# Performance work log

Measured on AMD Instinct MI355X. Metric: run time of the kernel, lower is better.

## Reference

```python
import jax, jax.numpy as jnp
import numpy as np


def setup_inputs() -> dict:
    key = jax.random.key(0)
    k1, k2 = jax.random.split(key)
    TOKENS, IN_F, OUT_F = 8192, 4096, 4096
    x = jax.random.normal(k1, (TOKENS, IN_F), dtype=jnp.float32)
    # kaiming_uniform_(a=sqrt(5)) then *2.0 -> roughly uniform in [-2/sqrt(in), 2/sqrt(in)]
    bound = 2.0 / np.sqrt(IN_F)
    weight = jax.random.uniform(k2, (OUT_F, IN_F), dtype=jnp.float32,
                                minval=-bound, maxval=bound)
    alpha = jnp.asarray(0.1, dtype=jnp.float32)
    bias = jnp.zeros((OUT_F,), dtype=jnp.float32)
    return {"x": x, "weight": weight, "alpha": alpha, "bias": bias, "bitwidth": 2}


def _quantize(W, alpha_eff, bitwidth):
    # alpha_eff > 0 scalar; W: [out, in]
    Wa = W / alpha_eff
    Wc = jnp.clip(Wa, -1.0, 1.0)
    if bitwidth == 1:
        Q = jnp.sign(Wc)
        Q = jnp.where(Q == 0, 1.0, Q)  # sign(0) -> +1
    elif bitwidth == 2:
        Q = jnp.where(jnp.abs(Wc) < 0.5, 0.0, jnp.sign(Wc))
    else:
        raise ValueError("bitwidth must be 1 or 2 here")
    return alpha_eff * Q


def reference(x, weight, alpha, bias, bitwidth):
    if bitwidth == 32:
        W_used = weight
    else:
        alpha_eff = jnp.abs(alpha) + 1e-8
        W_used = _quantize(weight, alpha_eff, bitwidth)
    # F.linear: x @ W^T + b
    return jnp.dot(x, W_used.T) + bias
```

## Files before the change

kernel.cpp:

```cpp
#include <hip/hip_runtime.h>


__global__ void qlin_row_flags(const float* __restrict__ W,
                               const float* __restrict__ alpha,
                               const int* __restrict__ bitwidth,
                               int* __restrict__ flags,
                               int IN_F) {
    const int row = blockIdx.x;
    const int bw = *bitwidth;
    __shared__ int s_any;
    if (threadIdx.x == 0) s_any = 0;
    __syncthreads();

    if (bw != 2) {
        if (threadIdx.x == 0) flags[row] = 1;
        return;
    }

    const float alpha_eff = fabsf(*alpha) + 1e-8f;
    bool any = false;

    const size_t base = (size_t)row * (size_t)IN_F;
    const int n4 = IN_F >> 2;
    const float4* Wrow4 = (const float4*)(W + base);
    for (int i = threadIdx.x; i < n4; i += blockDim.x) {
        float4 w = Wrow4[i];
        float ax = fabsf(fminf(1.f, fmaxf(-1.f, w.x / alpha_eff)));
        float ay = fabsf(fminf(1.f, fmaxf(-1.f, w.y / alpha_eff)));
        float az = fabsf(fminf(1.f, fmaxf(-1.f, w.z / alpha_eff)));
        float aw = fabsf(fminf(1.f, fmaxf(-1.f, w.w / alpha_eff)));
        any |= (ax >= 0.5f) | (ay >= 0.5f) | (az >= 0.5f) | (aw >= 0.5f);
    }
    for (int i = (n4 << 2) + threadIdx.x; i < IN_F; i += blockDim.x) {
        float a = fabsf(fminf(1.f, fmaxf(-1.f, W[base + i] / alpha_eff)));
        any |= (a >= 0.5f);
    }

    if (any) s_any = 1;
    __syncthreads();
    if (threadIdx.x == 0) flags[row] = s_any;
}

__global__ void qlin_output(const float* __restrict__ x,
                            const float* __restrict__ W,
                            const float* __restrict__ alpha,
                            const float* __restrict__ bias,
                            const int* __restrict__ bitwidth,
                            const int* __restrict__ flags,
                            float* __restrict__ y,
                            int TOKENS, int IN_F, int OUT_F) {
    const int per_tok_blocks = OUT_F >> 10;
    const int t  = blockIdx.x / per_tok_blocks;
    const int j0 = (blockIdx.x % per_tok_blocks) * 1024 + threadIdx.x * 4;
    if (t >= TOKENS || j0 + 3 >= OUT_F) return;

    const int4   f = *(const int4*)(flags + j0);
    const float4 b = *(const float4*)(bias + j0);
    float* yp = y + (size_t)t * (size_t)OUT_F + j0;

    if ((f.x | f.y | f.z | f.w) == 0) {
        *(float4*)yp = b;
        return;
    }

    const int bw = *bitwidth;
    const float alpha_eff = fabsf(*alpha) + 1e-8f;
    float acc[4] = {0.f, 0.f, 0.f, 0.f};
    const float* xr = x + (size_t)t * (size_t)IN_F;
    for (int i = 0; i < IN_F; ++i) {
        const float xv = xr[i];
#pragma unroll
        for (int c = 0; c < 4; ++c) {
            float w = W[(size_t)(j0 + c) * (size_t)IN_F + i];
            float wu;
            if (bw == 32) {
                wu = w;
            } else {
                float wa = fminf(1.f, fmaxf(-1.f, w / alpha_eff));
                float q;
                if (bw == 1) {
                    q = (wa >= 0.f) ? 1.f : -1.f;
                } else {
                    q = (fabsf(wa) < 0.5f) ? 0.f : ((wa > 0.f) ? 1.f : -1.f);
                }
                wu = alpha_eff * q;
            }
            acc[c] = fmaf(xv, wu, acc[c]);
        }
    }
    *(float4*)yp = make_float4(acc[0] + b.x, acc[1] + b.y,
                               acc[2] + b.z, acc[3] + b.w);
}

extern "C" void kernel_launch(void* const* d_in, const int* in_sizes, int n_in,
                              void* d_out, int out_size, void* d_ws, size_t ws_size,
                              hipStream_t stream) {
    const float* x     = (const float*)d_in[0];
    const float* W     = (const float*)d_in[1];
    const float* alpha = (const float*)d_in[2];
    const float* bias  = (const float*)d_in[3];
    const int*   bw    = (const int*)d_in[4];

    const int OUT_F  = in_sizes[3];
    const int IN_F   = in_sizes[1] / OUT_F;
    const int TOKENS = in_sizes[0] / IN_F;

    float* y = (float*)d_out;
    int* flags = (int*)d_ws;

    qlin_row_flags<<<OUT_F, 256, 0, stream>>>(W, alpha, bw, flags, IN_F);

    const int per_tok_blocks = OUT_F >> 10;
    dim3 grid(TOKENS * per_tok_blocks);
    qlin_output<<<grid, 256, 0, stream>>>(x, W, alpha, bias, bw, flags, y,
                                          TOKENS, IN_F, OUT_F);
}
```

Measured before the change: 243.6 us.

## Fuse row-flag scan and output pass into one column-blocked kernel

Merges the per-row zero-check kernel and the output kernel into a single launch. Each 1024-thread block scans 16 weight rows, keeps the flags in shared memory, then loops over all tokens to write either the bias or a dot product for those columns. The flag test now compares |w| against 0.5*alpha instead of dividing each weight, and the global flag workspace goes away. The cost is only 256 blocks with a serial scan-then-write phase, and output stores become 64-byte strided chunks per token row, which may weaken write coalescing.

Result: slower. 269.7 us (+10.7%).

```diff
diff --git a/kernel.cpp b/kernel.cpp
--- a/kernel.cpp
+++ b/kernel.cpp
@@ -1,95 +1,92 @@
 #include <hip/hip_runtime.h>
 
 
-__global__ void qlin_row_flags(const float* __restrict__ W,
-                               const float* __restrict__ alpha,
-                               const int* __restrict__ bitwidth,
-                               int* __restrict__ flags,
-                               int IN_F) {
-    const int row = blockIdx.x;
-    const int bw = *bitwidth;
-    __shared__ int s_any;
-    if (threadIdx.x == 0) s_any = 0;
+#define COLS_PER_BLOCK 16
+
+__global__ __launch_bounds__(1024) void qlin_fused(
+    const float* __restrict__ x,
+    const float* __restrict__ W,
+    const float* __restrict__ alpha,
+    const float* __restrict__ bias,
+    const int* __restrict__ bitwidth,
+    float* __restrict__ y,
+    int TOKENS, int IN_F, int OUT_F)
+{
+    const int j0  = blockIdx.x * COLS_PER_BLOCK;
+    const int tid = threadIdx.x;
+    const int bw  = *bitwidth;
+
+    __shared__ int s_flags[COLS_PER_BLOCK];
+
+    if (bw != 2) {
+        if (tid < COLS_PER_BLOCK) s_flags[tid] = 1;
+    } else {
+        if (tid < COLS_PER_BLOCK) s_flags[tid] = 0;
+        __syncthreads();
+        const float alpha_eff = fabsf(*alpha) + 1e-8f;
+        const float thr = 0.5f * alpha_eff;
+        const int n4 = IN_F >> 2;
+#pragma unroll
+        for (int k = 0; k < COLS_PER_BLOCK; ++k) {
+            const float4* Wrow = (const float4*)(W + (size_t)(j0 + k) * IN_F);
+            bool any = false;
+            for (int i = tid; i < n4; i += 1024) {
+                float4 w = Wrow[i];
+                any |= (fabsf(w.x) >= thr) | (fabsf(w.y) >= thr) |
+                       (fabsf(w.z) >= thr) | (fabsf(w.w) >= thr);
+            }
+            for (int i = (n4 << 2) + tid; i < IN_F; i += 1024)
+                any |= (fabsf(W[(size_t)(j0 + k) * IN_F + i]) >= thr);
+            if (any) s_flags[k] = 1;
+        }
+    }
     __syncthreads();
 
-    if (bw != 2) {
-        if (threadIdx.x == 0) flags[row] = 1;
-        return;
-    }
+    const int cg = tid & 3;
+    const int ts = tid >> 2;
+    const int c0 = cg << 2;
+    const int dense = s_flags[c0] | s_flags[c0 + 1] | s_flags[c0 + 2] | s_flags[c0 + 3];
+    const float4 bv = *(const float4*)(bias + j0 + c0);
 
-    const float alpha_eff = fabsf(*alpha) + 1e-8f;
-    bool any = false;
-
-    const size_t base = (size_t)row * (size_t)IN_F;
-    const int n4 = IN_F >> 2;
-    const float4* Wrow4 = (const float4*)(W + base);
-    for (int i = threadIdx.x; i < n4; i += blockDim.x) {
-        float4 w = Wrow4[i];
-        float ax = fabsf(fminf(1.f, fmaxf(-1.f, w.x / alpha_eff)));
-        float ay = fabsf(fminf(1.f, fmaxf(-1.f, w.y / alpha_eff)));
-        float az = fabsf(fminf(1.f, fmaxf(-1.f, w.z / alpha_eff)));
-        float aw = fabsf(fminf(1.f, fmaxf(-1.f, w.w / alpha_eff)));
-        any |= (ax >= 0.5f) | (ay >= 0.5f) | (az >= 0.5f) | (aw >= 0.5f);
-    }
-    for (int i = (n4 << 2) + threadIdx.x; i < IN_F; i += blockDim.x) {
-        float a = fabsf(fminf(1.f, fmaxf(-1.f, W[base + i] / alpha_eff)));
-        any |= (a >= 0.5f);
-    }
-
-    if (any) s_any = 1;
-    __syncthreads();
-    if (threadIdx.x == 0) flags[row] = s_any;
-}
-
-__global__ void qlin_output(const float* __restrict__ x,
-                            const float* __restrict__ W,
-                            const float* __restrict__ alpha,
-                            const float* __restrict__ bias,
-                            const int* __restrict__ bitwidth,
-                            const int* __restrict__ flags,
-                            float* __restrict__ y,
-                            int TOKENS, int IN_F, int OUT_F) {
-    const int per_tok_blocks = OUT_F >> 10;
-    const int t  = blockIdx.x / per_tok_blocks;
-    const int j0 = (blockIdx.x % per_tok_blocks) * 1024 + threadIdx.x * 4;
-    if (t >= TOKENS || j0 + 3 >= OUT_F) return;
-
-    const int4   f = *(const int4*)(flags + j0);
-    const float4 b = *(const float4*)(bias + j0);
-    float* yp = y + (size_t)t * (size_t)OUT_F + j0;
-
-    if ((f.x | f.y | f.z | f.w) == 0) {
-        *(float4*)yp = b;
-        return;
-    }
-
-    const int bw = *bitwidth;
-    const float alpha_eff = fabsf(*alpha) + 1e-8f;
-    float acc[4] = {0.f, 0.f, 0.f, 0.f};
-    const float* xr = x + (size_t)t * (size_t)IN_F;
-    for (int i = 0; i < IN_F; ++i) {
-        const float xv = xr[i];
+    if (!dense) {
+        for (int t0 = 0; t0 < TOKENS; t0 += 256) {
+            const int t = t0 + ts;
+            if (t < TOKENS)
+                *(float4*)(y + (size_t)t * OUT_F + j0 + c0) = bv;
+        }
+    } else {
+        const float alpha_eff = fabsf(*alpha) + 1e-8f;
+        for (int t0 = 0; t0 < TOKENS; t0 += 256) {
+            const int t = t0 + ts;
+            if (t >= TOKENS) continue;
+            const float* xr = x + (size_t)t * IN_F;
+            float acc[4] = {0.f, 0.f, 0.f, 0.f};
+            for (int i = 0; i < IN_F; ++i) {
+                const float xv = xr[i];
 #pragma unroll
-        for (int c = 0; c < 4; ++c) {
-            float w = W[(size_t)(j0 + c) * (size_t)IN_F + i];
-            float wu;
-            if (bw == 32) {
-                wu = w;
-            } else {
-                float wa = fminf(1.f, fmaxf(-1.f, w / alpha_eff));
-                float q;
-                if (bw == 1) {
-                    q = (wa >= 0.f) ? 1.f : -1.f;
-                } else {
-                    q = (fabsf(wa) < 0.5f) ? 0.f : ((wa > 0.f) ? 1.f : -1.f);
+                for (int c = 0; c < 4; ++c) {
+                    float w = W[(size_t)(j0 + c0 + c) * IN_F + i];
+                    float wu;
+                    if (bw == 32) {
+                        wu = w;
+                    } else {
+                        float wa = fminf(1.f, fmaxf(-1.f, w / alpha_eff));
+                        float q;
+                        if (bw == 1)
+                            q = (wa >= 0.f) ? 1.f : -1.f;
+                        else
+                            q = (fabsf(wa) < 0.5f) ? 0.f
+                                                   : ((wa > 0.f) ? 1.f : -1.f);
+                        wu = alpha_eff * q;
+                    }
+                    acc[c] = fmaf(xv, wu, acc[c]);
                 }
-                wu = alpha_eff * q;
             }
-            acc[c] = fmaf(xv, wu, acc[c]);
+            *(float4*)(y + (size_t)t * OUT_F + j0 + c0) =
+                make_float4(acc[0] + bv.x, acc[1] + bv.y,
+                            acc[2] + bv.z, acc[3] + bv.w);
         }
     }
-    *(float4*)yp = make_float4(acc[0] + b.x, acc[1] + b.y,
-                               acc[2] + b.z, acc[3] + b.w);
 }
 
 extern "C" void kernel_launch(void* const* d_in, const int* in_sizes, int n_in,
@@ -106,12 +103,8 @@
     const int TOKENS = in_sizes[0] / IN_F;
 
     float* y = (float*)d_out;
-    int* flags = (int*)d_ws;
 
-    qlin_row_flags<<<OUT_F, 256, 0, stream>>>(W, alpha, bw, flags, IN_F);
-
-    const int per_tok_blocks = OUT_F >> 10;
-    dim3 grid(TOKENS * per_tok_blocks);
-    qlin_output<<<grid, 256, 0, stream>>>(x, W, alpha, bias, bw, flags, y,
+    const int grid = OUT_F / COLS_PER_BLOCK;
+    qlin_fused<<<grid, 1024, 0, stream>>>(x, W, alpha, bias, bw, y,
                                           TOKENS, IN_F, OUT_F);
 }
```
